# Kernel tuning notes

Hardware: AMD Instinct MI355X
Metric: run time of the kernel (lower is better)

## Reference

```python
import jax, jax.numpy as jnp
import numpy as np

BS, N, F, G, H, L, HFC, C, E = 8, 15135, 64, 73, 256, 3, 512, 2, 242160

def setup_inputs() -> dict:
    key = jax.random.key(0)
    ks = jax.random.split(key, 16)
    s = 0.02
    return {
        "x": jax.random.normal(ks[0], (BS, N, F), jnp.float32),
        "batch": jnp.zeros((BS,), jnp.int64),
        "edge_index": jax.random.randint(ks[1], (2, E), 0, N, jnp.int64),
        "nodes_graphlets": jax.random.uniform(ks[2], (N, G), jnp.float32),
        "W1": jax.random.normal(ks[3], (F + G, H), jnp.float32) * s,
        "b1": jnp.zeros((H,), jnp.float32),
        "W2": jax.random.normal(ks[4], (H, H), jnp.float32) * s,
        "b2": jnp.zeros((H,), jnp.float32),
        "W3": jax.random.normal(ks[5], (H, H), jnp.float32) * s,
        "b3": jnp.zeros((H,), jnp.float32),
        "fc_W": jax.random.normal(ks[6], (L * H, 1), jnp.float32) * s,
        "fc_b": jnp.zeros((1,), jnp.float32),
        "lin1_W": jax.random.normal(ks[7], (N, HFC), jnp.float32) * s,
        "lin1_b": jnp.zeros((HFC,), jnp.float32),
        "lin2_W": jax.random.normal(ks[8], (HFC, C), jnp.float32) * s,
        "lin2_b": jnp.zeros((C,), jnp.float32),
    }


def reference(x, batch, edge_index, nodes_graphlets, W1, b1, W2, b2, W3, b3,
              fc_W, fc_b, lin1_W, lin1_b, lin2_W, lin2_b):
    bs, n, _ = x.shape
    row, col = edge_index[0], edge_index[1]
    # GCN normalization with self-loops (edge_weight = 1): D^-1/2 (A+I) D^-1/2
    deg = jnp.zeros((n,), x.dtype).at[col].add(1.0) + 1.0
    dis = jax.lax.rsqrt(deg)
    norm = dis[row] * dis[col]          # [E]
    deg_inv = 1.0 / deg                 # self-loop coefficient dis[i]^2

    def gcn_conv(h, W, b):
        hw = h @ W                                  # [bs, n, H]
        msg = hw[:, row, :] * norm[None, :, None]   # gather src, scale
        agg = jnp.zeros_like(hw).at[:, col, :].add(msg)
        agg = agg + hw * deg_inv[None, :, None]     # self loops
        return agg + b

    # graphlet_mode == 'input': concat graphlet features to node features
    pe = jnp.broadcast_to(nodes_graphlets[None], (bs,) + nodes_graphlets.shape)
    h = jnp.concatenate([x, pe], axis=2)            # [bs, n, F+G]

    h1 = jax.nn.elu(gcn_conv(h, W1, b1))
    h2 = jax.nn.elu(gcn_conv(h1, W2, b2))
    h3 = jax.nn.elu(gcn_conv(h2, W3, b3))

    # mode == 'cat': stack along new last dim then flatten (torch stack+view order)
    hc = jnp.stack([h1, h2, h3], axis=-1).reshape(bs, n, -1)  # [bs, n, H*L]
    g = (hc @ fc_W + fc_b).reshape(bs, n)                     # [bs, n_genes]

    z = jax.nn.elu(g @ lin1_W + lin1_b)   # dropout: eval mode -> identity
    out = z @ lin2_W + lin2_b
    return jax.nn.log_softmax(out, axis=-1)
```

## Files before the change

kernel.cpp:

```cpp
#include <hip/hip_runtime.h>
#include <hip/hip_bf16.h>

using bf16 = __hip_bfloat16;
typedef short s16x8 __attribute__((ext_vector_type(8)));
typedef short s16x4 __attribute__((ext_vector_type(4)));
typedef float f32x4 __attribute__((ext_vector_type(4)));
typedef float f32x2 __attribute__((ext_vector_type(2)));

#define BSZ   8
#define NN    15135
#define FF    64
#define GG    73
#define HH    256
#define EE    242160
#define K1P   160
#define MREAL (BSZ * NN)
#define MPAD  (946 * 128)
#define HFC   512
#define NCHUNK 64
#define NCHUNKS ((NN + NCHUNK - 1) / NCHUNK)
#define SCANB  ((NN + 255) / 256)
#define FP8_INV_SCALE 0.015625f

#define GLOAD_LDS16(gp, lp)                                                     \
    __builtin_amdgcn_global_load_lds(                                           \
        (const __attribute__((address_space(1))) void*)(gp),                    \
        (__attribute__((address_space(3))) void*)(lp), 16, 0, 0)

__device__ __forceinline__ unsigned char enc8(float v) {
    int p = __builtin_amdgcn_cvt_pk_fp8_f32(v, v, 0, false);
    return (unsigned char)(p & 0xff);
}

__global__ void k_deg(const int* __restrict__ col, int* __restrict__ cnt, int e) {
    int i = blockIdx.x * blockDim.x + threadIdx.x;
    if (i < e) atomicAdd(&cnt[col[i]], 1);
}

__global__ __launch_bounds__(256)
void k_scanA(const int* __restrict__ cnt, int* __restrict__ cursor,
             int* __restrict__ bsum) {
    __shared__ int ws[4];
    int i = blockIdx.x * 256 + threadIdx.x;
    int tid = threadIdx.x, lane = tid & 63, wid = tid >> 6;
    int v = (i < NN) ? cnt[i] : 0;
    int s = v;
    #pragma unroll
    for (int off = 1; off < 64; off <<= 1) {
        int t = __shfl_up(s, off);
        if (lane >= off) s += t;
    }
    if (lane == 63) ws[wid] = s;
    __syncthreads();
    int pre = 0;
    #pragma unroll
    for (int w = 0; w < 4; ++w) pre += (w < wid) ? ws[w] : 0;
    int incl = pre + s;
    if (i < NN) cursor[i] = incl;
    if (tid == 255) bsum[blockIdx.x] = incl;
}

__global__ __launch_bounds__(64)
void k_scanB(int* __restrict__ bsum, int* __restrict__ offs) {
    int t = threadIdx.x;
    int v = (t < SCANB) ? bsum[t] : 0;
    int s = v;
    #pragma unroll
    for (int off = 1; off < 64; off <<= 1) {
        int x = __shfl_up(s, off);
        if (t >= off) s += x;
    }
    if (t < SCANB) bsum[t] = s - v;
    if (t == 63) offs[NN] = s;
}

__global__ __launch_bounds__(256)
void k_scanC(const int* __restrict__ cnt, int* __restrict__ cursor,
             const int* __restrict__ bsum, int* __restrict__ offs,
             float* __restrict__ dis, float* __restrict__ dinv) {
    int i = blockIdx.x * 256 + threadIdx.x;
    if (i >= NN) return;
    int v = cnt[i];
    int excl = cursor[i] - v + bsum[blockIdx.x];
    offs[i] = excl;
    cursor[i] = excl;
    float d = (float)(v + 1);
    dis[i]  = rsqrtf(d);
    dinv[i] = (1.0f / d) * FP8_INV_SCALE;
}

__global__ void k_csr(const int* __restrict__ row, const int* __restrict__ col,
                      int* __restrict__ cursor, const float* __restrict__ dis,
                      int2* __restrict__ cpack, int e) {
    int i = blockIdx.x * blockDim.x + threadIdx.x;
    if (i >= e) return;
    int r = row[i], c = col[i];
    int p = atomicAdd(&cursor[c], 1);
    cpack[p] = make_int2(r, __float_as_int(dis[r] * dis[c] * FP8_INV_SCALE));
}

__global__ void k_prep_h0(const float* __restrict__ x, const float* __restrict__ gl,
                          bf16* __restrict__ h0) {
    int idx = blockIdx.x * blockDim.x + threadIdx.x;
    if (idx >= MREAL * (K1P / 8)) return;
    int m = idx / (K1P / 8);
    int q = idx - m * (K1P / 8);
    int j0 = q * 8;
    int n = m % NN;
    s16x8 o;
    #pragma unroll
    for (int k = 0; k < 8; ++k) {
        int j = j0 + k;
        float val;
        if (j < FF) val = x[(size_t)m * FF + j];
        else if (j < FF + GG) val = gl[(size_t)n * GG + (j - FF)];
        else val = 0.f;
        o[k] = (short)__bfloat16_as_ushort(__float2bfloat16(val));
    }
    *(s16x8*)&h0[(size_t)m * K1P + j0] = o;
}

__global__ void k_prep_w(const float* __restrict__ W, bf16* __restrict__ WT,
                         int K, int Kpad) {
    int idx = blockIdx.x * blockDim.x + threadIdx.x;
    if (idx >= 256 * Kpad) return;
    int nn = idx / Kpad, kk = idx - nn * Kpad;
    WT[idx] = __float2bfloat16(kk < K ? W[(size_t)kk * 256 + nn] : 0.f);
}

#define BK 32
template <int K>
__global__ __launch_bounds__(256)
void k_gemm(const bf16* __restrict__ A, const bf16* __restrict__ BT,
            unsigned char* __restrict__ C) {
    __shared__ __align__(16) short As[128 * BK];
    __shared__ __align__(16) short Bs[128 * BK];
    const int tid  = threadIdx.x;
    const int bm   = blockIdx.x * 128;
    const int bn   = blockIdx.y * 128;
    const int lane = tid & 63, wave = tid >> 6;
    const int wm   = (wave >> 1) * 64, wn = (wave & 1) * 64;
    const int fr   = lane & 15, quad = lane >> 4;
    const int r    = tid >> 2;
    const int c    = (tid & 3) * 8;

    const bf16* Ap0 = A  + (size_t)(bm + r) * K + c;
    const bf16* Ap1 = Ap0 + (size_t)64 * K;
    const bf16* Bp0 = BT + (size_t)(bn + r) * K + c;
    const bf16* Bp1 = Bp0 + (size_t)64 * K;
    short* AsT0 = As + tid * 8;
    short* AsT1 = As + 2048 + tid * 8;
    short* BsT0 = Bs + tid * 8;
    short* BsT1 = Bs + 2048 + tid * 8;

    f32x4 acc[4][4] = {};

    for (int k0 = 0; k0 < K; k0 += BK) {
        GLOAD_LDS16(Ap0 + k0, AsT0);
        GLOAD_LDS16(Ap1 + k0, AsT1);
        GLOAD_LDS16(Bp0 + k0, BsT0);
        GLOAD_LDS16(Bp1 + k0, BsT1);
        __syncthreads();
        s16x8 af[4], bfv[4];
        #pragma unroll
        for (int i = 0; i < 4; ++i)
            af[i] = *(const s16x8*)&As[(wm + i * 16 + fr) * BK + quad * 8];
        #pragma unroll
        for (int j = 0; j < 4; ++j)
            bfv[j] = *(const s16x8*)&Bs[(wn + j * 16 + fr) * BK + quad * 8];
        #pragma unroll
        for (int i = 0; i < 4; ++i)
            #pragma unroll
            for (int j = 0; j < 4; ++j)
                acc[i][j] = __builtin_amdgcn_mfma_f32_16x16x32_bf16(
                    af[i], bfv[j], acc[i][j], 0, 0, 0);
        __syncthreads();
    }

    #pragma unroll
    for (int i = 0; i < 4; ++i) {
        int rbase = bm + wm + i * 16 + quad * 4;
        #pragma unroll
        for (int rr = 0; rr < 4; ++rr) {
            int row = rbase + rr;
            if (row >= MREAL) continue;
            size_t co = (size_t)row * 256;
            #pragma unroll
            for (int j = 0; j < 4; ++j) {
                int colx = bn + wn + j * 16 + fr;
                C[co + colx] = enc8(acc[i][j][rr] * 64.f);
            }
        }
    }
}

#define AGG_GRP 512
#define AGG_STRIDE (AGG_GRP * 4)
__global__ __launch_bounds__(256)
void k_agg(const unsigned char* __restrict__ hw, bf16* __restrict__ hout,
           const int* __restrict__ offs, const int2* __restrict__ cpack,
           const float* __restrict__ dinv,
           const float* __restrict__ bias, const float* __restrict__ fcW,
           float* __restrict__ g, int writeH) {
    const int b    = blockIdx.x & 7;
    const int grp  = blockIdx.x >> 3;
    const int wid  = threadIdx.x >> 6;
    const int lane = threadIdx.x & 63;
    const int wv   = grp * 4 + wid;
    const unsigned c4 = lane * 4;

    const unsigned char* hwb = hw + (size_t)b * NN * 256;

    float bias4[4], fw4[4];
    #pragma unroll
    for (int k = 0; k < 4; ++k) {
        bias4[k] = bias[c4 + k];
        fw4[k]   = fcW[3 * (c4 + k)];
    }

    for (int v0 = wv; v0 < NN; v0 += AGG_STRIDE) {
        const int v   = __builtin_amdgcn_readfirstlane(v0);
        const int beg = __builtin_amdgcn_readfirstlane(offs[v]);
        const int end = __builtin_amdgcn_readfirstlane(offs[v + 1]);
        const float di = dinv[v];
        f32x2 a01, a23;
        {
            unsigned q = *(const unsigned*)(hwb + (((unsigned)v) << 8) + c4);
            f32x2 t0 = __builtin_amdgcn_cvt_pk_f32_fp8(q, false);
            f32x2 t1 = __builtin_amdgcn_cvt_pk_f32_fp8(q, true);
            f32x2 dd = {di, di};
            a01 = dd * t0;
            a23 = dd * t1;
        }

        #define EDGE1(qv, mv) {                                            \
            f32x2 t0 = __builtin_amdgcn_cvt_pk_f32_fp8((qv), false);       \
            f32x2 t1 = __builtin_amdgcn_cvt_pk_f32_fp8((qv), true);        \
            f32x2 mm = {(mv), (mv)};                                       \
            a01 += mm * t0;                                                \
            a23 += mm * t1; }

        int e = beg;
        while (e + 8 <= end) {
            int2 ep[8];
            #pragma unroll
            for (int u = 0; u < 8; ++u) ep[u] = cpack[e + u];
            unsigned q[8];
            #pragma unroll
            for (int u = 0; u < 8; ++u)
                q[u] = *(const unsigned*)(hwb + (((unsigned)ep[u].x) << 8) + c4);
            #pragma unroll
            for (int u = 0; u < 8; ++u) EDGE1(q[u], __int_as_float(ep[u].y));
            e += 8;
        }
        if (e + 4 <= end) {
            int2 ep[4];
            #pragma unroll
            for (int u = 0; u < 4; ++u) ep[u] = cpack[e + u];
            unsigned q[4];
            #pragma unroll
            for (int u = 0; u < 4; ++u)
                q[u] = *(const unsigned*)(hwb + (((unsigned)ep[u].x) << 8) + c4);
            #pragma unroll
            for (int u = 0; u < 4; ++u) EDGE1(q[u], __int_as_float(ep[u].y));
            e += 4;
        }
        if (e + 2 <= end) {
            int2 ep0 = cpack[e], ep1 = cpack[e + 1];
            unsigned q0 = *(const unsigned*)(hwb + (((unsigned)ep0.x) << 8) + c4);
            unsigned q1 = *(const unsigned*)(hwb + (((unsigned)ep1.x) << 8) + c4);
            EDGE1(q0, __int_as_float(ep0.y));
            EDGE1(q1, __int_as_float(ep1.y));
            e += 2;
        }
        if (e < end) {
            int2 ep0 = cpack[e];
            unsigned q0 = *(const unsigned*)(hwb + (((unsigned)ep0.x) << 8) + c4);
            EDGE1(q0, __int_as_float(ep0.y));
        }
        #undef EDGE1

        float acc4[4] = {a01[0], a01[1], a23[0], a23[1]};
        float p = 0.f;
        s16x4 o4;
        #pragma unroll
        for (int k = 0; k < 4; ++k) {
            float hv = acc4[k] + bias4[k];
            hv = hv > 0.f ? hv : (__expf(hv) - 1.0f);
            o4[k] = (short)__bfloat16_as_ushort(__float2bfloat16(hv));
            p += hv * fw4[k];
        }
        if (writeH)
            *(s16x4*)&hout[((size_t)b * NN + v) * 256 + c4] = o4;

        #pragma unroll
        for (int off = 32; off; off >>= 1) p += __shfl_xor(p, off);
        if (lane == 0) g[(size_t)b * NN + v] += p;
    }
}

__global__ __launch_bounds__(256)
void k_lin1(const float* __restrict__ g, const float* __restrict__ fcb,
            const float* __restrict__ W, float* __restrict__ zpart) {
    const int ny = blockIdx.x;
    const int n0 = ny * NCHUNK;
    const int cnt = min(NCHUNK, NN - n0);
    const int tid = threadIdx.x;
    __shared__ float sg[8][NCHUNK];
    float fb = fcb[0];
    for (int idx = tid; idx < 8 * NCHUNK; idx += 256) {
        int b = idx / NCHUNK, nn = idx - b * NCHUNK;
        sg[b][nn] = (nn < cnt) ? (g[(size_t)b * NN + n0 + nn] + fb) : 0.f;
    }
    __syncthreads();
    float2 acc[8] = {};
    for (int nn = 0; nn < cnt; ++nn) {
        float2 w = *(const float2*)&W[(size_t)(n0 + nn) * HFC + tid * 2];
        #pragma unroll
        for (int b = 0; b < 8; ++b) {
            float gv = sg[b][nn];
            acc[b].x += gv * w.x;
            acc[b].y += gv * w.y;
        }
    }
    #pragma unroll
    for (int b = 0; b < 8; ++b)
        *(float2*)&zpart[(size_t)ny * 4096 + b * 512 + tid * 2] = acc[b];
}

__global__ __launch_bounds__(256)
void k_lin1red(const float* __restrict__ zpart, float* __restrict__ zacc) {
    int t = blockIdx.x * 256 + threadIdx.x;
    float s = 0.f;
    for (int c = 0; c < NCHUNKS; ++c) s += zpart[(size_t)c * 4096 + t];
    zacc[t] = s;
}

__global__ __launch_bounds__(512)
void k_final(const float* __restrict__ zacc, const float* __restrict__ l1b,
             const float* __restrict__ W2, const float* __restrict__ l2b,
             float* __restrict__ out) {
    __shared__ float r0[512], r1[512];
    int t = threadIdx.x;
    for (int b = 0; b < 8; ++b) {
        float zv = zacc[b * HFC + t] + l1b[t];
        zv = zv > 0.f ? zv : (__expf(zv) - 1.0f);
        r0[t] = zv * W2[t * 2 + 0];
        r1[t] = zv * W2[t * 2 + 1];
        __syncthreads();
        for (int s = 256; s; s >>= 1) {
            if (t < s) { r0[t] += r0[t + s]; r1[t] += r1[t + s]; }
            __syncthreads();
        }
        if (t == 0) {
            float o0 = r0[0] + l2b[0], o1 = r1[0] + l2b[1];
            float m = fmaxf(o0, o1);
            float lse = m + logf(expf(o0 - m) + expf(o1 - m));
            out[b * 2 + 0] = o0 - lse;
            out[b * 2 + 1] = o1 - lse;
        }
        __syncthreads();
    }
}

extern "C" void kernel_launch(void* const* d_in, const int* in_sizes, int n_in,
                              void* d_out, int out_size, void* d_ws, size_t ws_size,
                              hipStream_t stream) {
    const float* x    = (const float*)d_in[0];
    const int*   eidx = (const int*)d_in[2];
    const float* gl   = (const float*)d_in[3];
    const float* W1   = (const float*)d_in[4];
    const float* b1   = (const float*)d_in[5];
    const float* W2   = (const float*)d_in[6];
    const float* b2   = (const float*)d_in[7];
    const float* W3   = (const float*)d_in[8];
    const float* b3   = (const float*)d_in[9];
    const float* fcW  = (const float*)d_in[10];
    const float* fcb  = (const float*)d_in[11];
    const float* l1W  = (const float*)d_in[12];
    const float* l1b  = (const float*)d_in[13];
    const float* l2W  = (const float*)d_in[14];
    const float* l2b  = (const float*)d_in[15];
    float* out = (float*)d_out;

    size_t off = 0;
    auto alloc = [&](size_t bytes) {
        void* p = (char*)d_ws + off;
        off += (bytes + 255) & ~(size_t)255;
        return p;
    };
    bf16* bufA          = (bf16*)alloc((size_t)MPAD * 256 * 2);
    unsigned char* bufC = (unsigned char*)alloc((size_t)MPAD * 256);
    bf16* W1T      = (bf16*)alloc(256 * K1P * 2);
    bf16* W2T      = (bf16*)alloc(256 * 256 * 2);
    bf16* W3T      = (bf16*)alloc(256 * 256 * 2);
    int*  deg_cnt  = (int*)alloc(NN * 4);
    int*  offs     = (int*)alloc((NN + 1) * 4);
    int*  cursor   = (int*)alloc(NN * 4);
    int*  bsum     = (int*)alloc(SCANB * 4);
    float* dis     = (float*)alloc(NN * 4);
    float* dinv    = (float*)alloc(NN * 4);
    int2* cpack    = (int2*)alloc((size_t)EE * 8);
    float* g       = (float*)alloc((size_t)BSZ * NN * 4);

    float* zpart = (float*)bufC;
    float* zacc  = (float*)(bufC + (8 << 20));

    hipMemsetAsync(deg_cnt, 0, NN * 4, stream);
    hipMemsetAsync(g, 0, (size_t)BSZ * NN * 4, stream);

    const int* erow = eidx;
    const int* ecol = eidx + EE;

    k_deg<<<(EE + 255) / 256, 256, 0, stream>>>(ecol, deg_cnt, EE);
    k_scanA<<<SCANB, 256, 0, stream>>>(deg_cnt, cursor, bsum);
    k_scanB<<<1, 64, 0, stream>>>(bsum, offs);
    k_scanC<<<SCANB, 256, 0, stream>>>(deg_cnt, cursor, bsum, offs, dis, dinv);
    k_csr<<<(EE + 255) / 256, 256, 0, stream>>>(erow, ecol, cursor, dis,
                                                cpack, EE);

    k_prep_h0<<<(MREAL * (K1P / 8) + 255) / 256, 256, 0, stream>>>(x, gl, bufA);
    k_prep_w<<<(256 * K1P + 255) / 256, 256, 0, stream>>>(W1, W1T, FF + GG, K1P);
    k_prep_w<<<(256 * 256 + 255) / 256, 256, 0, stream>>>(W2, W2T, 256, 256);
    k_prep_w<<<(256 * 256 + 255) / 256, 256, 0, stream>>>(W3, W3T, 256, 256);

    dim3 ggrid(MPAD / 128, 2);
    dim3 agrid(8 * AGG_GRP);

    k_gemm<K1P><<<ggrid, 256, 0, stream>>>(bufA, W1T, bufC);
    k_agg<<<agrid, 256, 0, stream>>>(bufC, bufA, offs, cpack, dinv,
                                     b1, fcW + 0, g, 1);
    k_gemm<256><<<ggrid, 256, 0, stream>>>(bufA, W2T, bufC);
    k_agg<<<agrid, 256, 0, stream>>>(bufC, bufA, offs, cpack, dinv,
                                     b2, fcW + 1, g, 1);
    k_gemm<256><<<ggrid, 256, 0, stream>>>(bufA, W3T, bufC);
    k_agg<<<agrid, 256, 0, stream>>>(bufC, bufA, offs, cpack, dinv,
                                     b3, fcW + 2, g, 0);

    k_lin1<<<NCHUNKS, 256, 0, stream>>>(g, fcb, l1W, zpart);
    k_lin1red<<<16, 256, 0, stream>>>(zpart, zacc);
    k_final<<<1, 512, 0, stream>>>(zacc, l1b, l2W, l2b, out);
}
```

Baseline: 477.9 us.

## Pack fp8 GEMM outputs into 32-bit stores using a permuted column layout

The GEMM epilogue converts four accumulator values to fp8 and writes them as one 32-bit word per row, replacing four scattered byte stores. This stores hidden columns in a permuted order. To keep results correct, the next layer's weight rows (W2, W3) are read through the same permutation, and the aggregation kernel maps its bias and fc weights accordingly. The aim is fewer, wider global stores, at the cost of index-remapping complexity across kernels.

```diff
diff --git a/kernel.cpp b/kernel.cpp
--- a/kernel.cpp
+++ b/kernel.cpp
@@ -27,9 +27,8 @@
         (const __attribute__((address_space(1))) void*)(gp),                    \
         (__attribute__((address_space(3))) void*)(lp), 16, 0, 0)
 
-__device__ __forceinline__ unsigned char enc8(float v) {
-    int p = __builtin_amdgcn_cvt_pk_fp8_f32(v, v, 0, false);
-    return (unsigned char)(p & 0xff);
+__device__ __forceinline__ int colmap(int p) {
+    return (p & 192) | ((p & 3) << 4) | ((p >> 2) & 15);
 }
 
 __global__ void k_deg(const int* __restrict__ col, int* __restrict__ cnt, int e) {
@@ -121,11 +120,12 @@
 }
 
 __global__ void k_prep_w(const float* __restrict__ W, bf16* __restrict__ WT,
-                         int K, int Kpad) {
+                         int K, int Kpad, int perm) {
     int idx = blockIdx.x * blockDim.x + threadIdx.x;
     if (idx >= 256 * Kpad) return;
     int nn = idx / Kpad, kk = idx - nn * Kpad;
-    WT[idx] = __float2bfloat16(kk < K ? W[(size_t)kk * 256 + nn] : 0.f);
+    int ks = perm ? colmap(kk) : kk;
+    WT[idx] = __float2bfloat16(kk < K ? W[(size_t)ks * 256 + nn] : 0.f);
 }
 
 #define BK 32
@@ -184,12 +184,11 @@
         for (int rr = 0; rr < 4; ++rr) {
             int row = rbase + rr;
             if (row >= MREAL) continue;
-            size_t co = (size_t)row * 256;
-            #pragma unroll
-            for (int j = 0; j < 4; ++j) {
-                int colx = bn + wn + j * 16 + fr;
-                C[co + colx] = enc8(acc[i][j][rr] * 64.f);
-            }
+            unsigned wpack = (unsigned)__builtin_amdgcn_cvt_pk_fp8_f32(
+                acc[i][0][rr] * 64.f, acc[i][1][rr] * 64.f, 0, false);
+            wpack = (unsigned)__builtin_amdgcn_cvt_pk_fp8_f32(
+                acc[i][2][rr] * 64.f, acc[i][3][rr] * 64.f, (int)wpack, true);
+            *(unsigned*)&C[(size_t)row * 256 + bn + wn + fr * 4] = wpack;
         }
     }
 }
@@ -214,8 +213,9 @@
     float bias4[4], fw4[4];
     #pragma unroll
     for (int k = 0; k < 4; ++k) {
-        bias4[k] = bias[c4 + k];
-        fw4[k]   = fcW[3 * (c4 + k)];
+        int cl = colmap((int)c4 + k);
+        bias4[k] = bias[cl];
+        fw4[k]   = fcW[3 * cl];
     }
 
     for (int v0 = wv; v0 < NN; v0 += AGG_STRIDE) {
@@ -420,9 +420,9 @@
                                                 cpack, EE);
 
     k_prep_h0<<<(MREAL * (K1P / 8) + 255) / 256, 256, 0, stream>>>(x, gl, bufA);
-    k_prep_w<<<(256 * K1P + 255) / 256, 256, 0, stream>>>(W1, W1T, FF + GG, K1P);
-    k_prep_w<<<(256 * 256 + 255) / 256, 256, 0, stream>>>(W2, W2T, 256, 256);
-    k_prep_w<<<(256 * 256 + 255) / 256, 256, 0, stream>>>(W3, W3T, 256, 256);
+    k_prep_w<<<(256 * K1P + 255) / 256, 256, 0, stream>>>(W1, W1T, FF + GG, K1P, 0);
+    k_prep_w<<<(256 * 256 + 255) / 256, 256, 0, stream>>>(W2, W2T, 256, 256, 1);
+    k_prep_w<<<(256 * 256 + 255) / 256, 256, 0, stream>>>(W3, W3T, 256, 256, 1);
 
     dim3 ggrid(MPAD / 128, 2);
     dim3 agrid(8 * AGG_GRP);
```

New measurement: 465.9 us. 2.5% less time.
